# Kernel optimization log

Hardware: AMD Instinct MI355X
Metric: run time of the kernel (lower is better)

The kernel has to match this reference:

```python
import jax, jax.numpy as jnp
import numpy as np

NH = 8  # num_heads
CHUNK = 32  # query-block size for chunked L1 cdist


def _mlp(x, w1, b1, w2, b2, w3, b3):
    h = jax.nn.relu(x @ w1 + b1)
    h = jax.nn.relu(h @ w2 + b2)
    return h @ w3 + b3


def _split_heads(x, nh):
    # Faithful to source: reshape last dim as (d, nh) then permute -> [B, nh, S, d]
    B, S, H = x.shape
    return jnp.transpose(x.reshape(B, S, H // nh, nh), (0, 3, 1, 2))


def _cdist_l1(K, Q, chunk=CHUNK):
    # torch.cdist(K, Q, p=1): D[b,h,i,j] = sum_d |K[b,h,i,d] - Q[b,h,j,d]|
    # Chunk over query rows to bound the broadcasted |K-Q| intermediate.
    B, h, Sq, d = Q.shape
    Sk = K.shape[2]
    Qb = jnp.moveaxis(Q.reshape(B, h, Sq // chunk, chunk, d), 2, 0)  # [nb,B,h,chunk,d]

    def block(q):  # q: [B,h,chunk,d]
        return jnp.sum(jnp.abs(K[:, :, :, None, :] - q[:, :, None, :, :]), axis=-1)  # [B,h,Sk,chunk]

    D = jax.lax.map(block, Qb)  # [nb,B,h,Sk,chunk]
    return jnp.moveaxis(D, 0, 3).reshape(B, h, Sk, Sq)


def setup_inputs() -> dict:
    key = jax.random.key(0)
    ks = jax.random.split(key, 32)
    B, S, F, H, O = 4, 1024, 128, 512, 128
    s = 0.02

    def lin(i, fin, fout):
        return (jax.random.normal(ks[i], (fin, fout), jnp.float32) * s,
                jnp.zeros((fout,), jnp.float32))

    inp = {
        'KEY': jax.random.normal(ks[0], (B, S, F), jnp.float32),
        'VALUE': jax.random.normal(ks[1], (B, S, F), jnp.float32),
        'QUERY': jax.random.normal(ks[2], (B, S, F), jnp.float32),
    }
    idx = 3
    for n in ['k', 'q', 'v']:
        for li, (fin, fout) in enumerate([(F, H), (H, H), (H, H)], 1):
            w, b = lin(idx, fin, fout); idx += 1
            inp[f'W{n}_w{li}'] = w
            inp[f'W{n}_b{li}'] = b
    w, b = lin(idx, H, O)
    inp['Wo_w'] = w
    inp['Wo_b'] = b
    return inp


def reference(KEY, VALUE, QUERY,
              Wk_w1, Wk_b1, Wk_w2, Wk_b2, Wk_w3, Wk_b3,
              Wq_w1, Wq_b1, Wq_w2, Wq_b2, Wq_w3, Wq_b3,
              Wv_w1, Wv_b1, Wv_w2, Wv_b2, Wv_w3, Wv_b3,
              Wo_w, Wo_b):
    Wk = _split_heads(_mlp(KEY, Wk_w1, Wk_b1, Wk_w2, Wk_b2, Wk_w3, Wk_b3), NH)   # [B,h,Sk,d]
    Wq = _split_heads(_mlp(QUERY, Wq_w1, Wq_b1, Wq_w2, Wq_b2, Wq_w3, Wq_b3), NH)  # [B,h,Sq,d]
    Wv = _split_heads(_mlp(VALUE, Wv_w1, Wv_b1, Wv_w2, Wv_b2, Wv_w3, Wv_b3), NH)  # [B,h,Sk,d]

    D = _cdist_l1(Wk, Wq)                              # [B,h,Sk,Sq]
    attn = jax.nn.softmax(-(D * D) * 0.5, axis=1)      # softmax over HEAD axis, as in source
    out = jnp.einsum('bhik,bhij->bhjk', attn, Wv)      # [B,h,d,Sq]
    B, h, d, Sq = out.shape
    out = jnp.transpose(out, (0, 2, 1, 3)).reshape(B, d * h, Sq)  # [B,hidden,Sq]
    out = jnp.transpose(out, (0, 2, 1))                # [B,Sq,hidden]
    return out @ Wo_w + Wo_b                           # dropout = identity (eval)
```

## Files before the change

kernel.cpp:

```cpp
#include <hip/hip_runtime.h>
#include <hip/hip_bf16.h>
#include <hip/hip_fp16.h>

typedef unsigned short u16;
typedef __attribute__((ext_vector_type(8))) short short8;
typedef __attribute__((ext_vector_type(4))) float floatx4;

#define DEVI static __device__ __forceinline__

DEVI float bf2f(u16 b) { return __uint_as_float(((unsigned)b) << 16); }
DEVI u16 f2bf(float f) {
  __hip_bfloat16 h = __float2bfloat16(f);
  u16 u; __builtin_memcpy(&u, &h, 2); return u;
}
DEVI u16 f2h(float f) {
  __half h = __float2half(f);
  u16 u; __builtin_memcpy(&u, &h, 2); return u;
}

DEVI void async_ld16(const u16* g, u16* l) {
  __builtin_amdgcn_global_load_lds(
      (const __attribute__((address_space(1))) unsigned int*)g,
      (__attribute__((address_space(3))) unsigned int*)l, 16, 0, 0);
}

template <int CTRL>
DEVI float dpp_add_f(float v) {
  int i; __builtin_memcpy(&i, &v, 4);
  int p = __builtin_amdgcn_update_dpp(0, i, CTRL, 0xF, 0xF, false);
  float pv; __builtin_memcpy(&pv, &p, 4);
  return v + pv;
}

DEVI int hperm(int f) { return ((f & 7) << 6) | (f >> 3); }

struct H4 { __half2 a, b, c, d; };
DEVI H4 toH4(const int4 v) { H4 r; __builtin_memcpy(&r, &v, 16); return r; }
DEVI int4 fromH4(const H4 x) { int4 r; __builtin_memcpy(&r, &x, 16); return r; }

struct TransArgs {
  const float* src[10];
  u16* dst[10];
  int R[10];
  int C[10];
};

__global__ __launch_bounds__(256) void transpose_k(TransArgs t) {
  const int z = blockIdx.z;
  const float* __restrict__ src = t.src[z];
  u16* __restrict__ dst = t.dst[z];
  const int R = t.R[z], C = t.C[z];
  const int c0 = blockIdx.x * 32, r0 = blockIdx.y * 32;
  if (c0 >= C || r0 >= R) return;
  __shared__ float tile[32][33];
  const int tx = threadIdx.x & 31, ty = threadIdx.x >> 5;
  for (int i = ty; i < 32; i += 8)
    tile[i][tx] = src[(size_t)(r0 + i) * C + c0 + tx];
  __syncthreads();
  for (int i = ty; i < 32; i += 8) {
    const int f = r0 + tx;
    const int fi = (z == 9) ? hperm(f) : f;
    dst[(size_t)(c0 + i) * R + fi] = f2bf(tile[tx][i]);
  }
}

struct ConvArgs {
  const float* src[3];
  u16* dst[3];
};

__global__ __launch_bounds__(256) void conv_k(ConvArgs c) {
  const int z = blockIdx.z;
  const float* __restrict__ src = c.src[z];
  u16* __restrict__ dst = c.dst[z];
  const size_t i = ((size_t)blockIdx.x * 256 + threadIdx.x) * 8;
  const float4 f0 = *(const float4*)(src + i);
  const float4 f1 = *(const float4*)(src + i + 4);
  u16 tmp[8] = {f2bf(f0.x), f2bf(f0.y), f2bf(f0.z), f2bf(f0.w),
                f2bf(f1.x), f2bf(f1.y), f2bf(f1.z), f2bf(f1.w)};
  int4 t; __builtin_memcpy(&t, tmp, 16);
  *(int4*)(dst + i) = t;
}

struct GemmArgs {
  const u16* A[3];
  const u16* WT[3];
  const float* bias[3];
  void* C[3];
};

__global__ __launch_bounds__(256, 3) void gemm128(GemmArgs ga, int M, int N, int K,
                                                  int relu, int c_mode, int out_perm) {
  const int z = blockIdx.z;
  const u16* __restrict__ A = ga.A[z];
  const u16* __restrict__ WT = ga.WT[z];
  const float* __restrict__ bias = ga.bias[z];
  void* __restrict__ C = ga.C[z];

  __shared__ u16 As[128 * 64];
  __shared__ u16 Bs[128 * 64];

  const int tid = threadIdx.x;
  const int lane = tid & 63;
  const int wave = tid >> 6;
  const int wm = wave >> 1, wn = wave & 1;
  const int mb = blockIdx.y, nb = blockIdx.x;

  floatx4 acc[4][4];
#pragma unroll
  for (int mi = 0; mi < 4; ++mi)
#pragma unroll
    for (int ni = 0; ni < 4; ++ni) acc[mi][ni] = floatx4{0.f, 0.f, 0.f, 0.f};

  const int g = (lane & 7) ^ ((lane >> 3) & 7);
  const int srow = lane >> 3;
  const size_t aRowBase = (size_t)(mb * 128 + wave * 32 + srow) * K + g * 8;
  const size_t bRowBase = (size_t)(nb * 128 + wave * 32 + srow) * K + g * 8;

  for (int k0 = 0; k0 < K; k0 += 64) {
    __syncthreads();
#pragma unroll
    for (int it = 0; it < 4; ++it) {
      async_ld16(A + aRowBase + (size_t)it * 8 * K + k0, As + (wave * 32 + it * 8) * 64);
      async_ld16(WT + bRowBase + (size_t)it * 8 * K + k0, Bs + (wave * 32 + it * 8) * 64);
    }
    __syncthreads();
#pragma unroll
    for (int ks = 0; ks < 2; ++ks) {
      const int phys = ((ks * 4 + (lane >> 4)) ^ (lane & 7)) * 8;
      short8 af[4], bf[4];
#pragma unroll
      for (int i = 0; i < 4; ++i) {
        const int m = wm * 64 + i * 16 + (lane & 15);
        const int n = wn * 64 + i * 16 + (lane & 15);
        af[i] = *(const short8*)(As + m * 64 + phys);
        bf[i] = *(const short8*)(Bs + n * 64 + phys);
      }
#pragma unroll
      for (int mi = 0; mi < 4; ++mi)
#pragma unroll
        for (int ni = 0; ni < 4; ++ni)
          acc[mi][ni] = __builtin_amdgcn_mfma_f32_16x16x32_bf16(af[mi], bf[ni], acc[mi][ni], 0, 0, 0);
    }
  }

#pragma unroll
  for (int mi = 0; mi < 4; ++mi)
#pragma unroll
    for (int ni = 0; ni < 4; ++ni) {
      const int col = nb * 128 + wn * 64 + ni * 16 + (lane & 15);
      const float bv = bias[col];
      const int colw = out_perm ? hperm(col) : col;
      const floatx4 v = acc[mi][ni];
#pragma unroll
      for (int r = 0; r < 4; ++r) {
        const int row = mb * 128 + wm * 64 + mi * 16 + (lane >> 4) * 4 + r;
        float x = v[r] + bv;
        if (relu) x = fmaxf(x, 0.f);
        if (c_mode == 1)      ((float*)C)[(size_t)row * N + colw] = x;
        else if (c_mode == 2) ((u16*)C)[(size_t)row * N + colw] = f2h(x);
        else                  ((u16*)C)[(size_t)row * N + colw] = f2bf(x);
      }
    }
}

__global__ __launch_bounds__(256, 3) void attn_kernel(const u16* __restrict__ Km,
                                                      const u16* __restrict__ Qm,
                                                      const u16* __restrict__ Vm,
                                                      u16* __restrict__ partial) {
  __shared__ alignas(16) u16 lds[4 * 4096];

  const int tid = threadIdx.x;
  const int lane = tid & 63;
  const int wave = tid >> 6;
  const int wid = blockIdx.x * 4 + wave;
  const int qt = wid & 63;
  const int sp = (wid >> 6) & 15;
  const int b = wid >> 10;
  const int j0 = qt * 16;

  const int qg = lane >> 4;
  const int h = (lane >> 1) & 7;
  const int half = lane & 1;

  int grans[4];
#pragma unroll
  for (int pi = 0; pi < 4; ++pi)
    grans[pi] = h * 8 + half * 4 + ((pi + h) & 3);

  H4 Qh[4][4];
#pragma unroll
  for (int qi = 0; qi < 4; ++qi) {
    const u16* qrow = Qm + (size_t)(b * 1024 + j0 + qg + qi * 4) * 512;
#pragma unroll
    for (int pi = 0; pi < 4; ++pi)
      Qh[qi][pi] = toH4(*(const int4*)(qrow + grans[pi] * 8));
  }

  const __half2 z2 = __float2half2_rn(0.f);
  H4 o[4][4];
#pragma unroll
  for (int qi = 0; qi < 4; ++qi)
#pragma unroll
    for (int pi = 0; pi < 4; ++pi) { o[qi][pi].a = z2; o[qi][pi].b = z2; o[qi][pi].c = z2; o[qi][pi].d = z2; }

  const int keyBase = b * 1024 + sp * 64;
  const u16* kgb = Km + (size_t)keyBase * 512 + lane * 8;
  const u16* vgb = Vm + (size_t)keyBase * 512 + lane * 8;
  u16* wbase = lds + wave * 4096;

  async_ld16(kgb, wbase);
  async_ld16(kgb + 512, wbase + 512);
  async_ld16(vgb, wbase + 1024);
  async_ld16(vgb + 512, wbase + 1536);

#pragma unroll 1
  for (int cc = 0; cc < 32; ++cc) {
    asm volatile("s_waitcnt vmcnt(0)" ::: "memory");
    __builtin_amdgcn_sched_barrier(0);
    const int cur = cc & 1;
    const u16* buf = wbase + cur * 2048;
    if (cc < 31) {
      const u16* kg = kgb + (size_t)(cc + 1) * 1024;
      const u16* vg = vgb + (size_t)(cc + 1) * 1024;
      u16* nb = wbase + (cur ^ 1) * 2048;
      async_ld16(kg, nb);
      async_ld16(kg + 512, nb + 512);
      async_ld16(vg, nb + 1024);
      async_ld16(vg + 512, nb + 1536);
    }

    __half2 A0[2][4], A1[2][4];
#pragma unroll
    for (int r = 0; r < 2; ++r) {
      const u16* krow = buf + r * 512;
#pragma unroll
      for (int qi = 0; qi < 4; ++qi) { A0[r][qi] = z2; A1[r][qi] = z2; }
#pragma unroll
      for (int pi = 0; pi < 4; ++pi) {
        const H4 k4 = toH4(*(const int4*)(krow + grans[pi] * 8));
#pragma unroll
        for (int qi = 0; qi < 4; ++qi) {
          A0[r][qi] = __hadd2(A0[r][qi], __habs2(__hsub2(k4.a, Qh[qi][pi].a)));
          A1[r][qi] = __hadd2(A1[r][qi], __habs2(__hsub2(k4.b, Qh[qi][pi].b)));
          A0[r][qi] = __hadd2(A0[r][qi], __habs2(__hsub2(k4.c, Qh[qi][pi].c)));
          A1[r][qi] = __hadd2(A1[r][qi], __habs2(__hsub2(k4.d, Qh[qi][pi].d)));
        }
      }
    }

    __half2 wh[2][4];
#pragma unroll
    for (int r = 0; r < 2; ++r)
#pragma unroll
      for (int qi = 0; qi < 4; ++qi) {
        const __half2 s2 = __hadd2(A0[r][qi], A1[r][qi]);
        float d8p = __half2float(__low2half(s2)) + __half2float(__high2half(s2));
        const float d8 = dpp_add_f<0xB1>(d8p);
        const float e = __expf(-0.5f * d8 * d8);
        float nrm = e;
        nrm = dpp_add_f<0x4E>(nrm);
        nrm = dpp_add_f<0x141>(nrm);
        nrm = dpp_add_f<0x140>(nrm);
        const float w = e * __builtin_amdgcn_rcpf(nrm);
        wh[r][qi] = __float2half2_rn(w);
      }

#pragma unroll
    for (int r = 0; r < 2; ++r) {
      const u16* vrow = buf + 1024 + r * 512;
#pragma unroll
      for (int pi = 0; pi < 4; ++pi) {
        const H4 v4 = toH4(*(const int4*)(vrow + grans[pi] * 8));
#pragma unroll
        for (int qi = 0; qi < 4; ++qi) {
          o[qi][pi].a = __hfma2(wh[r][qi], v4.a, o[qi][pi].a);
          o[qi][pi].b = __hfma2(wh[r][qi], v4.b, o[qi][pi].b);
          o[qi][pi].c = __hfma2(wh[r][qi], v4.c, o[qi][pi].c);
          o[qi][pi].d = __hfma2(wh[r][qi], v4.d, o[qi][pi].d);
        }
      }
    }
  }

  u16* Ew = wbase;
#pragma unroll
  for (int qi = 0; qi < 4; ++qi) {
#pragma unroll
    for (int pi = 0; pi < 4; ++pi)
      *(int4*)(Ew + qg * 512 + grans[pi] * 8) = fromH4(o[qi][pi]);
    asm volatile("s_waitcnt lgkmcnt(0)" ::: "memory");
#pragma unroll
    for (int p = 0; p < 4; ++p) {
      const int4 v = *(const int4*)(Ew + p * 512 + lane * 8);
      u16* dst = partial + (size_t)sp * (4096 * 512) + (size_t)(b * 1024 + j0 + p + qi * 4) * 512;
      *(int4*)(dst + lane * 8) = v;
    }
    asm volatile("s_waitcnt lgkmcnt(0)" ::: "memory");
  }
}

__global__ __launch_bounds__(256, 3) void gemm_final(const u16* __restrict__ P,
                                                     const u16* __restrict__ WT9,
                                                     const float* __restrict__ bias,
                                                     float* __restrict__ out) {
  __shared__ u16 As[128 * 64];
  __shared__ u16 Bs[128 * 64];

  const int tid = threadIdx.x;
  const int lane = tid & 63;
  const int wave = tid >> 6;
  const int wm = wave >> 1, wn = wave & 1;
  const int mb = blockIdx.y;
  const int kc = blockIdx.x;
  const int k0 = kc * 64;

  const int g = (lane & 7) ^ ((lane >> 3) & 7);
  const int srow = lane >> 3;

  const size_t bRowBase = (size_t)(wave * 32 + srow) * 512 + g * 8;
#pragma unroll
  for (int it = 0; it < 4; ++it)
    async_ld16(WT9 + bRowBase + (size_t)it * 8 * 512 + k0, Bs + (wave * 32 + it * 8) * 64);

#pragma unroll
  for (int it = 0; it < 4; ++it) {
    const size_t gaddr = (size_t)(mb * 128 + wave * 32 + it * 8 + srow) * 512 + k0 + g * 8;
    float s[8] = {0.f, 0.f, 0.f, 0.f, 0.f, 0.f, 0.f, 0.f};
#pragma unroll
    for (int sp = 0; sp < 16; ++sp) {
      const int4 t = *(const int4*)(P + (size_t)sp * (4096 * 512) + gaddr);
      const __half* th = reinterpret_cast<const __half*>(&t);
#pragma unroll
      for (int j = 0; j < 8; ++j) s[j] += __half2float(th[j]);
    }
    u16 tmp[8];
#pragma unroll
    for (int j = 0; j < 8; ++j) tmp[j] = f2bf(s[j]);
    int4 pk; __builtin_memcpy(&pk, tmp, 16);
    *(int4*)(As + (wave * 32 + it * 8) * 64 + lane * 8) = pk;
  }
  __syncthreads();

  floatx4 acc[4][4];
#pragma unroll
  for (int mi = 0; mi < 4; ++mi)
#pragma unroll
    for (int ni = 0; ni < 4; ++ni) acc[mi][ni] = floatx4{0.f, 0.f, 0.f, 0.f};

#pragma unroll
  for (int ks = 0; ks < 2; ++ks) {
    const int phys = ((ks * 4 + (lane >> 4)) ^ (lane & 7)) * 8;
    short8 af[4], bf[4];
#pragma unroll
    for (int i = 0; i < 4; ++i) {
      const int m = wm * 64 + i * 16 + (lane & 15);
      const int n = wn * 64 + i * 16 + (lane & 15);
      af[i] = *(const short8*)(As + m * 64 + phys);
      bf[i] = *(const short8*)(Bs + n * 64 + phys);
    }
#pragma unroll
    for (int mi = 0; mi < 4; ++mi)
#pragma unroll
      for (int ni = 0; ni < 4; ++ni)
        acc[mi][ni] = __builtin_amdgcn_mfma_f32_16x16x32_bf16(af[mi], bf[ni], acc[mi][ni], 0, 0, 0);
  }

#pragma unroll
  for (int mi = 0; mi < 4; ++mi)
#pragma unroll
    for (int ni = 0; ni < 4; ++ni) {
      const int col = wn * 64 + ni * 16 + (lane & 15);
      const float bv = (kc == 0) ? bias[col] : 0.f;
      const floatx4 v = acc[mi][ni];
#pragma unroll
      for (int r = 0; r < 4; ++r) {
        const int row = mb * 128 + wm * 64 + mi * 16 + (lane >> 4) * 4 + r;
        atomicAdd(&out[(size_t)row * 128 + col], v[r] + bv);
      }
    }
}

extern "C" void kernel_launch(void* const* d_in, const int* in_sizes, int n_in,
                              void* d_out, int out_size, void* d_ws, size_t ws_size,
                              hipStream_t stream) {
  (void)in_sizes; (void)n_in; (void)out_size; (void)ws_size;
  char* wsp = (char*)d_ws;
  size_t off = 0;
  auto take = [&](size_t bytes) {
    void* p = (void*)(wsp + off);
    off += ((bytes + 255) & ~(size_t)255);
    return p;
  };

  static const int wR[10] = {128, 512, 512, 128, 512, 512, 128, 512, 512, 512};
  static const int wC[10] = {512, 512, 512, 512, 512, 512, 512, 512, 512, 128};
  static const int widx[10] = {3, 5, 7, 9, 11, 13, 15, 17, 19, 21};

  u16* WT[10];
  for (int i = 0; i < 10; ++i) WT[i] = (u16*)take((size_t)wR[i] * wC[i] * 2);
  u16* a0[3]; for (int i = 0; i < 3; ++i) a0[i] = (u16*)take((size_t)4096 * 128 * 2);
  u16* h1[3]; for (int i = 0; i < 3; ++i) h1[i] = (u16*)take((size_t)4096 * 512 * 2);
  u16* h2[3]; for (int i = 0; i < 3; ++i) h2[i] = (u16*)take((size_t)4096 * 512 * 2);
  u16* partial = (u16*)take((size_t)16 * 4096 * 512 * 2);

  TransArgs ta;
  for (int i = 0; i < 10; ++i) {
    ta.src[i] = (const float*)d_in[widx[i]];
    ta.dst[i] = WT[i];
    ta.R[i] = wR[i];
    ta.C[i] = wC[i];
  }
  hipLaunchKernelGGL(transpose_k, dim3(16, 16, 10), dim3(256), 0, stream, ta);

  ConvArgs ca;
  ca.src[0] = (const float*)d_in[0]; ca.src[1] = (const float*)d_in[2]; ca.src[2] = (const float*)d_in[1];
  ca.dst[0] = a0[0]; ca.dst[1] = a0[1]; ca.dst[2] = a0[2];
  hipLaunchKernelGGL(conv_k, dim3(256, 1, 3), dim3(256), 0, stream, ca);

  GemmArgs g1 = {};
  for (int i = 0; i < 3; ++i) g1.A[i] = a0[i];
  g1.WT[0] = WT[0]; g1.WT[1] = WT[3]; g1.WT[2] = WT[6];
  g1.bias[0] = (const float*)d_in[4]; g1.bias[1] = (const float*)d_in[10]; g1.bias[2] = (const float*)d_in[16];
  g1.C[0] = h1[0]; g1.C[1] = h1[1]; g1.C[2] = h1[2];
  hipLaunchKernelGGL(gemm128, dim3(4, 32, 3), dim3(256), 0, stream, g1, 4096, 512, 128, 1, 0, 0);

  GemmArgs g2 = {};
  for (int i = 0; i < 3; ++i) { g2.A[i] = h1[i]; g2.C[i] = h2[i]; }
  g2.WT[0] = WT[1]; g2.WT[1] = WT[4]; g2.WT[2] = WT[7];
  g2.bias[0] = (const float*)d_in[6]; g2.bias[1] = (const float*)d_in[12]; g2.bias[2] = (const float*)d_in[18];
  hipLaunchKernelGGL(gemm128, dim3(4, 32, 3), dim3(256), 0, stream, g2, 4096, 512, 512, 1, 0, 0);

  GemmArgs g3 = {};
  for (int i = 0; i < 3; ++i) { g3.A[i] = h2[i]; g3.C[i] = (void*)h1[i]; }
  g3.WT[0] = WT[2]; g3.WT[1] = WT[5]; g3.WT[2] = WT[8];
  g3.bias[0] = (const float*)d_in[8]; g3.bias[1] = (const float*)d_in[14]; g3.bias[2] = (const float*)d_in[20];
  hipLaunchKernelGGL(gemm128, dim3(4, 32, 3), dim3(256), 0, stream, g3, 4096, 512, 512, 0, 2, 1);

  hipLaunchKernelGGL(attn_kernel, dim3(1024), dim3(256), 0, stream, h1[0], h1[1], h1[2], partial);

  hipMemsetAsync(d_out, 0, (size_t)4096 * 128 * sizeof(float), stream);
  hipLaunchKernelGGL(gemm_final, dim3(8, 32), dim3(256), 0, stream,
                     partial, WT[9], (const float*)d_in[22], (float*)d_out);
}
```

Before: 364.9 us.

## Fuse input conversion and three-layer MLP into one kernel per row tile

Replaces the separate fp32-to-bf16 conversion kernel and three GEMM launches with a single kernel that processes a 32-row tile through all three MLP layers. Intermediate activations stay in swizzled LDS instead of round-tripping through global memory. Weight fragments are read directly from global/L2 without LDS staging. Only 384 blocks are launched, each re-reading the full weight matrices, which lowers parallelism and raises L2 weight traffic.

```diff
diff --git a/kernel.cpp b/kernel.cpp
--- a/kernel.cpp
+++ b/kernel.cpp
@@ -64,104 +64,179 @@
   }
 }
 
-struct ConvArgs {
-  const float* src[3];
-  u16* dst[3];
+struct MlpArgs {
+  const float* X[3];
+  const u16* W1[3];
+  const u16* W2[3];
+  const u16* W3[3];
+  const float* b1[3];
+  const float* b2[3];
+  const float* b3[3];
+  u16* Y[3];
 };
 
-__global__ __launch_bounds__(256) void conv_k(ConvArgs c) {
+__global__ __launch_bounds__(512, 2) void mlp3_k(MlpArgs ma) {
+  __shared__ u16 hA[32 * 128];
+  __shared__ u16 hS[32 * 512];
+
   const int z = blockIdx.z;
-  const float* __restrict__ src = c.src[z];
-  u16* __restrict__ dst = c.dst[z];
-  const size_t i = ((size_t)blockIdx.x * 256 + threadIdx.x) * 8;
-  const float4 f0 = *(const float4*)(src + i);
-  const float4 f1 = *(const float4*)(src + i + 4);
-  u16 tmp[8] = {f2bf(f0.x), f2bf(f0.y), f2bf(f0.z), f2bf(f0.w),
-                f2bf(f1.x), f2bf(f1.y), f2bf(f1.z), f2bf(f1.w)};
-  int4 t; __builtin_memcpy(&t, tmp, 16);
-  *(int4*)(dst + i) = t;
-}
-
-struct GemmArgs {
-  const u16* A[3];
-  const u16* WT[3];
-  const float* bias[3];
-  void* C[3];
-};
-
-__global__ __launch_bounds__(256, 3) void gemm128(GemmArgs ga, int M, int N, int K,
-                                                  int relu, int c_mode, int out_perm) {
-  const int z = blockIdx.z;
-  const u16* __restrict__ A = ga.A[z];
-  const u16* __restrict__ WT = ga.WT[z];
-  const float* __restrict__ bias = ga.bias[z];
-  void* __restrict__ C = ga.C[z];
-
-  __shared__ u16 As[128 * 64];
-  __shared__ u16 Bs[128 * 64];
-
+  const int r0 = blockIdx.x * 32;
   const int tid = threadIdx.x;
   const int lane = tid & 63;
   const int wave = tid >> 6;
-  const int wm = wave >> 1, wn = wave & 1;
-  const int mb = blockIdx.y, nb = blockIdx.x;
-
-  floatx4 acc[4][4];
-#pragma unroll
-  for (int mi = 0; mi < 4; ++mi)
+  const int colBase = wave * 64;
+  const int l15 = lane & 15;
+  const int lq = lane >> 4;
+
+  {
+    const int rr = tid >> 4, gg = tid & 15;
+    const int g0 = gg ^ (rr & 7);
+    const float* src = ma.X[z] + (size_t)(r0 + rr) * 128 + g0 * 8;
+    const float4 f0 = *(const float4*)(src);
+    const float4 f1 = *(const float4*)(src + 4);
+    u16 tmp[8] = {f2bf(f0.x), f2bf(f0.y), f2bf(f0.z), f2bf(f0.w),
+                  f2bf(f1.x), f2bf(f1.y), f2bf(f1.z), f2bf(f1.w)};
+    int4 t; __builtin_memcpy(&t, tmp, 16);
+    *(int4*)(hA + rr * 128 + gg * 8) = t;
+  }
+  __syncthreads();
+
+  floatx4 acc[2][4];
+#pragma unroll
+  for (int mi = 0; mi < 2; ++mi)
 #pragma unroll
     for (int ni = 0; ni < 4; ++ni) acc[mi][ni] = floatx4{0.f, 0.f, 0.f, 0.f};
 
-  const int g = (lane & 7) ^ ((lane >> 3) & 7);
-  const int srow = lane >> 3;
-  const size_t aRowBase = (size_t)(mb * 128 + wave * 32 + srow) * K + g * 8;
-  const size_t bRowBase = (size_t)(nb * 128 + wave * 32 + srow) * K + g * 8;
-
-  for (int k0 = 0; k0 < K; k0 += 64) {
-    __syncthreads();
-#pragma unroll
-    for (int it = 0; it < 4; ++it) {
-      async_ld16(A + aRowBase + (size_t)it * 8 * K + k0, As + (wave * 32 + it * 8) * 64);
-      async_ld16(WT + bRowBase + (size_t)it * 8 * K + k0, Bs + (wave * 32 + it * 8) * 64);
-    }
-    __syncthreads();
-#pragma unroll
-    for (int ks = 0; ks < 2; ++ks) {
-      const int phys = ((ks * 4 + (lane >> 4)) ^ (lane & 7)) * 8;
-      short8 af[4], bf[4];
-#pragma unroll
-      for (int i = 0; i < 4; ++i) {
-        const int m = wm * 64 + i * 16 + (lane & 15);
-        const int n = wn * 64 + i * 16 + (lane & 15);
-        af[i] = *(const short8*)(As + m * 64 + phys);
-        bf[i] = *(const short8*)(Bs + n * 64 + phys);
-      }
-#pragma unroll
-      for (int mi = 0; mi < 4; ++mi)
+  {
+    const u16* __restrict__ W1 = ma.W1[z];
+#pragma unroll
+    for (int kk = 0; kk < 4; ++kk) {
+      const int gk = kk * 4 + lq;
+      short8 af[2], bf[4];
+#pragma unroll
+      for (int mi = 0; mi < 2; ++mi) {
+        const int m = mi * 16 + l15;
+        af[mi] = *(const short8*)(hA + m * 128 + (gk ^ (m & 7)) * 8);
+      }
+#pragma unroll
+      for (int ni = 0; ni < 4; ++ni) {
+        const int col = colBase + ni * 16 + l15;
+        bf[ni] = *(const short8*)(W1 + (size_t)col * 128 + gk * 8);
+      }
+#pragma unroll
+      for (int mi = 0; mi < 2; ++mi)
 #pragma unroll
         for (int ni = 0; ni < 4; ++ni)
           acc[mi][ni] = __builtin_amdgcn_mfma_f32_16x16x32_bf16(af[mi], bf[ni], acc[mi][ni], 0, 0, 0);
     }
-  }
-
-#pragma unroll
-  for (int mi = 0; mi < 4; ++mi)
-#pragma unroll
-    for (int ni = 0; ni < 4; ++ni) {
-      const int col = nb * 128 + wn * 64 + ni * 16 + (lane & 15);
-      const float bv = bias[col];
-      const int colw = out_perm ? hperm(col) : col;
-      const floatx4 v = acc[mi][ni];
-#pragma unroll
-      for (int r = 0; r < 4; ++r) {
-        const int row = mb * 128 + wm * 64 + mi * 16 + (lane >> 4) * 4 + r;
-        float x = v[r] + bv;
-        if (relu) x = fmaxf(x, 0.f);
-        if (c_mode == 1)      ((float*)C)[(size_t)row * N + colw] = x;
-        else if (c_mode == 2) ((u16*)C)[(size_t)row * N + colw] = f2h(x);
-        else                  ((u16*)C)[(size_t)row * N + colw] = f2bf(x);
-      }
-    }
+    const float* __restrict__ b1 = ma.b1[z];
+#pragma unroll
+    for (int mi = 0; mi < 2; ++mi)
+#pragma unroll
+      for (int ni = 0; ni < 4; ++ni) {
+        const int col = colBase + ni * 16 + l15;
+        const float bv = b1[col];
+        const floatx4 v = acc[mi][ni];
+#pragma unroll
+        for (int r = 0; r < 4; ++r) {
+          const int row = mi * 16 + lq * 4 + r;
+          const float x = fmaxf(v[r] + bv, 0.f);
+          hS[row * 512 + (((col >> 3) ^ (row & 7)) * 8) + (col & 7)] = f2bf(x);
+        }
+      }
+  }
+  __syncthreads();
+
+#pragma unroll
+  for (int mi = 0; mi < 2; ++mi)
+#pragma unroll
+    for (int ni = 0; ni < 4; ++ni) acc[mi][ni] = floatx4{0.f, 0.f, 0.f, 0.f};
+  {
+    const u16* __restrict__ W2 = ma.W2[z];
+#pragma unroll
+    for (int kk = 0; kk < 16; ++kk) {
+      const int gk = kk * 4 + lq;
+      short8 af[2], bf[4];
+#pragma unroll
+      for (int mi = 0; mi < 2; ++mi) {
+        const int m = mi * 16 + l15;
+        af[mi] = *(const short8*)(hS + m * 512 + (gk ^ (m & 7)) * 8);
+      }
+#pragma unroll
+      for (int ni = 0; ni < 4; ++ni) {
+        const int col = colBase + ni * 16 + l15;
+        bf[ni] = *(const short8*)(W2 + (size_t)col * 512 + gk * 8);
+      }
+#pragma unroll
+      for (int mi = 0; mi < 2; ++mi)
+#pragma unroll
+        for (int ni = 0; ni < 4; ++ni)
+          acc[mi][ni] = __builtin_amdgcn_mfma_f32_16x16x32_bf16(af[mi], bf[ni], acc[mi][ni], 0, 0, 0);
+    }
+  }
+  __syncthreads();
+  {
+    const float* __restrict__ b2 = ma.b2[z];
+#pragma unroll
+    for (int mi = 0; mi < 2; ++mi)
+#pragma unroll
+      for (int ni = 0; ni < 4; ++ni) {
+        const int col = colBase + ni * 16 + l15;
+        const float bv = b2[col];
+        const floatx4 v = acc[mi][ni];
+#pragma unroll
+        for (int r = 0; r < 4; ++r) {
+          const int row = mi * 16 + lq * 4 + r;
+          const float x = fmaxf(v[r] + bv, 0.f);
+          hS[row * 512 + (((col >> 3) ^ (row & 7)) * 8) + (col & 7)] = f2bf(x);
+        }
+      }
+  }
+  __syncthreads();
+
+#pragma unroll
+  for (int mi = 0; mi < 2; ++mi)
+#pragma unroll
+    for (int ni = 0; ni < 4; ++ni) acc[mi][ni] = floatx4{0.f, 0.f, 0.f, 0.f};
+  {
+    const u16* __restrict__ W3 = ma.W3[z];
+#pragma unroll
+    for (int kk = 0; kk < 16; ++kk) {
+      const int gk = kk * 4 + lq;
+      short8 af[2], bf[4];
+#pragma unroll
+      for (int mi = 0; mi < 2; ++mi) {
+        const int m = mi * 16 + l15;
+        af[mi] = *(const short8*)(hS + m * 512 + (gk ^ (m & 7)) * 8);
+      }
+#pragma unroll
+      for (int ni = 0; ni < 4; ++ni) {
+        const int col = colBase + ni * 16 + l15;
+        bf[ni] = *(const short8*)(W3 + (size_t)col * 512 + gk * 8);
+      }
+#pragma unroll
+      for (int mi = 0; mi < 2; ++mi)
+#pragma unroll
+        for (int ni = 0; ni < 4; ++ni)
+          acc[mi][ni] = __builtin_amdgcn_mfma_f32_16x16x32_bf16(af[mi], bf[ni], acc[mi][ni], 0, 0, 0);
+    }
+    const float* __restrict__ b3 = ma.b3[z];
+    u16* __restrict__ Y = ma.Y[z];
+#pragma unroll
+    for (int mi = 0; mi < 2; ++mi)
+#pragma unroll
+      for (int ni = 0; ni < 4; ++ni) {
+        const int col = colBase + ni * 16 + l15;
+        const float bv = b3[col];
+        const int colw = hperm(col);
+        const floatx4 v = acc[mi][ni];
+#pragma unroll
+        for (int r = 0; r < 4; ++r) {
+          const int row = mi * 16 + lq * 4 + r;
+          Y[(size_t)(r0 + row) * 512 + colw] = f2h(v[r] + bv);
+        }
+      }
+  }
 }
 
 __global__ __launch_bounds__(256, 3) void attn_kernel(const u16* __restrict__ Km,
@@ -399,9 +474,7 @@
 
   u16* WT[10];
   for (int i = 0; i < 10; ++i) WT[i] = (u16*)take((size_t)wR[i] * wC[i] * 2);
-  u16* a0[3]; for (int i = 0; i < 3; ++i) a0[i] = (u16*)take((size_t)4096 * 128 * 2);
   u16* h1[3]; for (int i = 0; i < 3; ++i) h1[i] = (u16*)take((size_t)4096 * 512 * 2);
-  u16* h2[3]; for (int i = 0; i < 3; ++i) h2[i] = (u16*)take((size_t)4096 * 512 * 2);
   u16* partial = (u16*)take((size_t)16 * 4096 * 512 * 2);
 
   TransArgs ta;
@@ -413,29 +486,20 @@
   }
   hipLaunchKernelGGL(transpose_k, dim3(16, 16, 10), dim3(256), 0, stream, ta);
 
-  ConvArgs ca;
-  ca.src[0] = (const float*)d_in[0]; ca.src[1] = (const float*)d_in[2]; ca.src[2] = (const float*)d_in[1];
-  ca.dst[0] = a0[0]; ca.dst[1] = a0[1]; ca.dst[2] = a0[2];
-  hipLaunchKernelGGL(conv_k, dim3(256, 1, 3), dim3(256), 0, stream, ca);
-
-  GemmArgs g1 = {};
-  for (int i = 0; i < 3; ++i) g1.A[i] = a0[i];
-  g1.WT[0] = WT[0]; g1.WT[1] = WT[3]; g1.WT[2] = WT[6];
-  g1.bias[0] = (const float*)d_in[4]; g1.bias[1] = (const float*)d_in[10]; g1.bias[2] = (const float*)d_in[16];
-  g1.C[0] = h1[0]; g1.C[1] = h1[1]; g1.C[2] = h1[2];
-  hipLaunchKernelGGL(gemm128, dim3(4, 32, 3), dim3(256), 0, stream, g1, 4096, 512, 128, 1, 0, 0);
-
-  GemmArgs g2 = {};
-  for (int i = 0; i < 3; ++i) { g2.A[i] = h1[i]; g2.C[i] = h2[i]; }
-  g2.WT[0] = WT[1]; g2.WT[1] = WT[4]; g2.WT[2] = WT[7];
-  g2.bias[0] = (const float*)d_in[6]; g2.bias[1] = (const float*)d_in[12]; g2.bias[2] = (const float*)d_in[18];
-  hipLaunchKernelGGL(gemm128, dim3(4, 32, 3), dim3(256), 0, stream, g2, 4096, 512, 512, 1, 0, 0);
-
-  GemmArgs g3 = {};
-  for (int i = 0; i < 3; ++i) { g3.A[i] = h2[i]; g3.C[i] = (void*)h1[i]; }
-  g3.WT[0] = WT[2]; g3.WT[1] = WT[5]; g3.WT[2] = WT[8];
-  g3.bias[0] = (const float*)d_in[8]; g3.bias[1] = (const float*)d_in[14]; g3.bias[2] = (const float*)d_in[20];
-  hipLaunchKernelGGL(gemm128, dim3(4, 32, 3), dim3(256), 0, stream, g3, 4096, 512, 512, 0, 2, 1);
+  MlpArgs ma;
+  ma.X[0] = (const float*)d_in[0];
+  ma.X[1] = (const float*)d_in[2];
+  ma.X[2] = (const float*)d_in[1];
+  for (int i = 0; i < 3; ++i) {
+    ma.W1[i] = WT[3 * i];
+    ma.W2[i] = WT[3 * i + 1];
+    ma.W3[i] = WT[3 * i + 2];
+    ma.Y[i] = h1[i];
+  }
+  ma.b1[0] = (const float*)d_in[4];  ma.b2[0] = (const float*)d_in[6];  ma.b3[0] = (const float*)d_in[8];
+  ma.b1[1] = (const float*)d_in[10]; ma.b2[1] = (const float*)d_in[12]; ma.b3[1] = (const float*)d_in[14];
+  ma.b1[2] = (const float*)d_in[16]; ma.b2[2] = (const float*)d_in[18]; ma.b3[2] = (const float*)d_in[20];
+  hipLaunchKernelGGL(mlp3_k, dim3(128, 1, 3), dim3(512), 0, stream, ma);
 
   hipLaunchKernelGGL(attn_kernel, dim3(1024), dim3(256), 0, stream, h1[0], h1[1], h1[2], partial);
 
```

Measured after the change: 385.4 us. 1.06x slower.
